# Performance work log

Hardware: AMD Instinct MI355X
Metric: run time of the kernel (lower is better)

## Reference

```python
import jax, jax.numpy as jnp
import numpy as np

N_SAMPLES = 524288
N_FEATURES = 64
N_GATES = 64
N_OUTPUTS = 8
BASE = N_FEATURES + 2                # X cols + constant-0 col + constant-1 col
MAX_CONN = BASE + N_GATES            # 130
TEMPERATURE = 1.0                    # forward() default
NEG = -1e9                           # mask value for not-yet-available slots


def setup_inputs() -> dict:
    key = jax.random.key(0)
    k1, k2, k3 = jax.random.split(key, 3)
    X = jax.random.uniform(k1, (N_SAMPLES, N_FEATURES), dtype=jnp.float32)
    gate_weights = jax.random.normal(k2, (N_GATES, MAX_CONN), dtype=jnp.float32) * 0.1
    output_weights = jax.random.normal(k3, (N_GATES, N_OUTPUTS), dtype=jnp.float32) * 0.1
    output_scale = jnp.ones((N_OUTPUTS,), dtype=jnp.float32)
    return {"X": X, "gate_weights": gate_weights,
            "output_weights": output_weights, "output_scale": output_scale}


def reference(X, gate_weights, output_weights, output_scale):
    n = X.shape[0]
    # available = [X | zeros | ones | gate slots]; gate slots filled sequentially
    buf = jnp.concatenate([
        X,
        jnp.zeros((n, 1), X.dtype),
        jnp.ones((n, 1), X.dtype),
        jnp.zeros((n, N_GATES), X.dtype),
    ], axis=1)                                            # [N, MAX_CONN]

    # Connection selection is data-independent: softmax over the first
    # (BASE + gate_idx) slots of each gate's weight row, then top-2.
    col_ids = jnp.arange(MAX_CONN)
    avail_mask = col_ids[None, :] < (BASE + jnp.arange(N_GATES))[:, None]
    logits = jnp.where(avail_mask, gate_weights / TEMPERATURE, NEG)
    probs = jax.nn.softmax(logits, axis=1)                # [n_gates, MAX_CONN]
    _, top2 = jax.lax.top_k(probs, 2)                     # [n_gates, 2]

    # Sequential NAND chain over a small fixed number of gates (structural loop).
    gate_outs = []
    for i in range(N_GATES):
        a = buf[:, top2[i, 0]]                            # [N]
        b = buf[:, top2[i, 1]]
        g = 1.0 - a * b                                   # continuous NAND
        gate_outs.append(g)
        buf = buf.at[:, BASE + i].set(g)

    gate_matrix = jnp.stack(gate_outs, axis=1)            # [N, n_gates]
    outputs = (gate_matrix @ output_weights) * output_scale
    return outputs
```

## Files before the change

kernel.cpp:

```cpp
#include <hip/hip_runtime.h>
#include <hip/hip_fp16.h>

#define N_SAMPLES 524288
#define N_FEATURES 64
#define N_GATES 64
#define N_OUTPUTS 8
#define BASE_COLS 66
#define MAX_CONN 130
#define NCOLS 131

#define TPB 256
#define NW 128
#define STR 129

#define WS_GIDX   0
#define WS_NCHK   512
#define WS_OWH2   1024
#define WS_ENT    4096

__device__ inline void top2_ins(float x, int j, float& v1, int& i1, float& v2, int& i2) {
    bool gt1 = (x > v1) || (x == v1 && j < i1);
    bool gt2 = (x > v2) || (x == v2 && j < i2);
    if (gt1) { v2 = v1; i2 = i1; v1 = x; i1 = j; }
    else if (gt2) { v2 = x; i2 = j; }
}

__global__ __launch_bounds__(64) void topk_prep_kernel(const float* __restrict__ gw,
                                                       int2* __restrict__ gidx) {
    const int i = blockIdx.x;
    const int l = threadIdx.x;
    const float* w = gw + i * MAX_CONN;
    const int avail = BASE_COLS + i;

    float v1 = -1e30f, v2 = -1e30f;
    int   i1 = 0x7fffffff, i2 = 0x7fffffff;
    for (int s = 0; s < 3; ++s) {
        int j = l + 64 * s;
        if (j < avail) top2_ins(w[j], j, v1, i1, v2, i2);
    }
    #pragma unroll
    for (int d = 1; d < 64; d <<= 1) {
        float ov1 = __shfl_xor(v1, d);
        int   oi1 = __shfl_xor(i1, d);
        float ov2 = __shfl_xor(v2, d);
        int   oi2 = __shfl_xor(i2, d);
        top2_ins(ov1, oi1, v1, i1, v2, i2);
        top2_ins(ov2, oi2, v1, i1, v2, i2);
    }
    if (l == 0) gidx[i] = make_int2(i1, i2);
}

__global__ __launch_bounds__(64) void plan_kernel(const int2* __restrict__ gidx,
                                                  const float* __restrict__ ow,
                                                  char* __restrict__ ws) {
    __shared__ int spa[N_GATES], spb[N_GATES];
    const int t = threadIdx.x;

    unsigned int* owh = (unsigned int*)(ws + WS_OWH2);
    int4* ent = (int4*)(ws + WS_ENT);
    int*  nchk = (int*)(ws + WS_NCHK);

    int2 p = gidx[t];
    spa[t] = p.x; spb[t] = p.y;

    #pragma unroll
    for (int o = 0; o < N_OUTPUTS; ++o) {
        unsigned short u = __half_as_ushort(__float2half(ow[t * N_OUTPUTS + o]));
        owh[t * N_OUTPUTS + o] = (unsigned int)u * 0x10001u;
    }
    if (t < N_OUTPUTS) owh[N_GATES * N_OUTPUTS + t] = 0u;

    __syncthreads();

    if (t == 0) {
        int i = 0, e = 0;
        while (i < N_GATES) {
            int cs = i;
            int limit = BASE_COLS + cs;
            while (i < N_GATES && spa[i] < limit && spb[i] < limit) ++i;
            for (int j = cs; j < i; ++j)
                ent[e++] = make_int4(spa[j] * STR, spb[j] * STR,
                                     (BASE_COLS + j) * STR, j);
            while (e & 7)
                ent[e++] = make_int4(64 * STR, 64 * STR, 130 * STR, N_GATES);
        }
        *nchk = e >> 3;
    }
}

__global__ __launch_bounds__(NW) void circuit_kernel(
    const float* __restrict__ X,
    const char*  __restrict__ ws,
    const float* __restrict__ scale,
    float*       __restrict__ out)
{
    __shared__ __half2 buf[NCOLS * STR];

    const int t = threadIdx.x;
    const long long s0 = (long long)blockIdx.x * TPB;

    const int4* ent = (const int4*)(ws + WS_ENT);
    const unsigned int* owh = (const unsigned int*)(ws + WS_OWH2);
    const int nc = *(const int*)(ws + WS_NCHK);

    const float4* Xv = (const float4*)(X + s0 * N_FEATURES);
    #pragma unroll
    for (int k = 0; k < 16; ++k) {
        int q  = k * NW + t;
        int c4 = q & 15;
        int j  = q >> 4;
        float4 va = Xv[(2 * j)     * 16 + c4];
        float4 vb = Xv[(2 * j + 1) * 16 + c4];
        int c = 4 * c4;
        buf[(c + 0) * STR + j] = __halves2half2(__float2half(va.x), __float2half(vb.x));
        buf[(c + 1) * STR + j] = __halves2half2(__float2half(va.y), __float2half(vb.y));
        buf[(c + 2) * STR + j] = __halves2half2(__float2half(va.z), __float2half(vb.z));
        buf[(c + 3) * STR + j] = __halves2half2(__float2half(va.w), __float2half(vb.w));
    }
    buf[64 * STR + t] = __halves2half2(__float2half(0.0f), __float2half(0.0f));
    buf[65 * STR + t] = __halves2half2(__float2half(1.0f), __float2half(1.0f));
    __syncthreads();

    const __half2 one2 = __halves2half2(__float2half(1.0f), __float2half(1.0f));
    __half2 acc[N_OUTPUTS];
    #pragma unroll
    for (int o = 0; o < N_OUTPUTS; ++o) acc[o] = __halves2half2(__float2half(0.0f), __float2half(0.0f));

    for (int c = 0; c < nc; ++c) {
        int4 E[8];
        #pragma unroll
        for (int j = 0; j < 8; ++j) E[j] = ent[c * 8 + j];

        __half2 av[8], bv[8];
        #pragma unroll
        for (int j = 0; j < 8; ++j) {
            av[j] = buf[E[j].x + t];
            bv[j] = buf[E[j].y + t];
        }
        __half2 gv[8];
        #pragma unroll
        for (int j = 0; j < 8; ++j) {
            gv[j] = __hfma2(__hneg2(av[j]), bv[j], one2);
            buf[E[j].z + t] = gv[j];
        }
        #pragma unroll
        for (int j = 0; j < 8; ++j) {
            const __half2* wrow = (const __half2*)(owh + E[j].w * N_OUTPUTS);
            #pragma unroll
            for (int o = 0; o < N_OUTPUTS; ++o)
                acc[o] = __hfma2(gv[j], wrow[o], acc[o]);
        }
    }

    float sc[N_OUTPUTS];
    #pragma unroll
    for (int o = 0; o < N_OUTPUTS; ++o) sc[o] = scale[o];

    float a0[N_OUTPUTS], a1[N_OUTPUTS];
    #pragma unroll
    for (int o = 0; o < N_OUTPUTS; ++o) {
        a0[o] = __low2float(acc[o])  * sc[o];
        a1[o] = __high2float(acc[o]) * sc[o];
    }
    float4* outv = (float4*)(out + (s0 + 2 * t) * N_OUTPUTS);
    outv[0] = make_float4(a0[0], a0[1], a0[2], a0[3]);
    outv[1] = make_float4(a0[4], a0[5], a0[6], a0[7]);
    outv[2] = make_float4(a1[0], a1[1], a1[2], a1[3]);
    outv[3] = make_float4(a1[4], a1[5], a1[6], a1[7]);
}

extern "C" void kernel_launch(void* const* d_in, const int* in_sizes, int n_in,
                              void* d_out, int out_size, void* d_ws, size_t ws_size,
                              hipStream_t stream) {
    const float* X     = (const float*)d_in[0];
    const float* gw    = (const float*)d_in[1];
    const float* ow    = (const float*)d_in[2];
    const float* scale = (const float*)d_in[3];
    float* out = (float*)d_out;

    char* ws = (char*)d_ws;
    int2* gidx = (int2*)(ws + WS_GIDX);

    topk_prep_kernel<<<N_GATES, 64, 0, stream>>>(gw, gidx);
    plan_kernel<<<1, 64, 0, stream>>>(gidx, ow, ws);

    int blocks = N_SAMPLES / TPB;
    circuit_kernel<<<blocks, NW, 0, stream>>>(X, ws, scale, out);
}
```

Baseline: 240.9 us.

## Compact LDS via liveness-based row allocation and prefetch chunk entries

The planner now reference-counts each column and assigns shared-memory rows only to live values. It reuses freed rows for later gate outputs and sends dead outputs to a scratch row, which shrinks the LDS footprint from 131 rows to 77 and should allow more resident blocks per CU. Unused X columns are skipped during staging. The circuit loop also double-buffers the next chunk's entry descriptors so their loads overlap the current chunk, at the cost of extra registers and a fixed row cap that could overflow if more values are live at once.

New measurement: 285.4 us. 18.5% more time.

```diff
diff --git a/kernel.cpp b/kernel.cpp
--- a/kernel.cpp
+++ b/kernel.cpp
@@ -7,16 +7,21 @@
 #define N_OUTPUTS 8
 #define BASE_COLS 66
 #define MAX_CONN 130
-#define NCOLS 131
 
 #define TPB 256
 #define NW 128
 #define STR 129
 
-#define WS_GIDX   0
-#define WS_NCHK   512
-#define WS_OWH2   1024
-#define WS_ENT    4096
+#define CAP_ROWS 77
+#define SCRATCH_ROW (CAP_ROWS - 1)
+#define DYN_LDS (CAP_ROWS * STR * 4)
+
+#define WS_GIDX 0
+#define WS_NCHK 1024
+#define WS_CROW 1056
+#define WS_XMAP 2048
+#define WS_OWH2 4096
+#define WS_ENT  8192
 
 __device__ inline void top2_ins(float x, int j, float& v1, int& i1, float& v2, int& i2) {
     bool gt1 = (x > v1) || (x == v1 && j < i1);
@@ -53,15 +58,13 @@
 __global__ __launch_bounds__(64) void plan_kernel(const int2* __restrict__ gidx,
                                                   const float* __restrict__ ow,
                                                   char* __restrict__ ws) {
-    __shared__ int spa[N_GATES], spb[N_GATES];
+    __shared__ int ga[N_GATES], gb[N_GATES];
+    __shared__ int refcnt[MAX_CONN], cmap[MAX_CONN];
     const int t = threadIdx.x;
 
     unsigned int* owh = (unsigned int*)(ws + WS_OWH2);
-    int4* ent = (int4*)(ws + WS_ENT);
-    int*  nchk = (int*)(ws + WS_NCHK);
-
     int2 p = gidx[t];
-    spa[t] = p.x; spb[t] = p.y;
+    ga[t] = p.x; gb[t] = p.y;
 
     #pragma unroll
     for (int o = 0; o < N_OUTPUTS; ++o) {
@@ -70,21 +73,48 @@
     }
     if (t < N_OUTPUTS) owh[N_GATES * N_OUTPUTS + t] = 0u;
 
+    refcnt[t] = 0; refcnt[t + 64] = 0;
+    cmap[t] = -1;  cmap[t + 64] = -1;
+    if (t < 2) { refcnt[128 + t] = 0; cmap[128 + t] = -1; }
     __syncthreads();
 
     if (t == 0) {
-        int i = 0, e = 0;
+        for (int i = 0; i < N_GATES; ++i) { refcnt[ga[i]]++; refcnt[gb[i]]++; }
+
+        int frees[CAP_ROWS]; int nfree = 0;
+        for (int r = SCRATCH_ROW - 1; r >= 0; --r) frees[nfree++] = r;
+
+        refcnt[64] += 1000000;
+        cmap[64] = frees[--nfree];
+        if (refcnt[65] > 0) cmap[65] = frees[--nfree];
+        for (int c = 0; c < 64; ++c) if (refcnt[c] > 0) cmap[c] = frees[--nfree];
+
+        int* xmap = (int*)(ws + WS_XMAP);
+        for (int c = 0; c < 64; ++c) xmap[c] = (cmap[c] >= 0) ? cmap[c] * STR : -1;
+        *(int2*)(ws + WS_CROW) =
+            make_int2(cmap[64] * STR, (cmap[65] >= 0) ? cmap[65] * STR : -1);
+
+        int4* ent = (int4*)(ws + WS_ENT);
+        const int zoff = cmap[64] * STR;
+        int e = 0, i = 0;
         while (i < N_GATES) {
-            int cs = i;
-            int limit = BASE_COLS + cs;
-            while (i < N_GATES && spa[i] < limit && spb[i] < limit) ++i;
-            for (int j = cs; j < i; ++j)
-                ent[e++] = make_int4(spa[j] * STR, spb[j] * STR,
-                                     (BASE_COLS + j) * STR, j);
-            while (e & 7)
-                ent[e++] = make_int4(64 * STR, 64 * STR, 130 * STR, N_GATES);
-        }
-        *nchk = e >> 3;
+            int cs = i, limit = BASE_COLS + cs;
+            while (i < N_GATES && ga[i] < limit && gb[i] < limit) ++i;
+            for (int j = cs; j < i; ++j) {
+                int ca = ga[j], cb = gb[j];
+                int ra = cmap[ca] * STR, rb = cmap[cb] * STR;
+                if (--refcnt[ca] == 0 && nfree < SCRATCH_ROW) frees[nfree++] = cmap[ca];
+                if (--refcnt[cb] == 0 && nfree < SCRATCH_ROW) frees[nfree++] = cmap[cb];
+                int ro = SCRATCH_ROW;
+                if (refcnt[BASE_COLS + j] > 0 && nfree > 0) ro = frees[--nfree];
+                cmap[BASE_COLS + j] = ro;
+                ent[e++] = make_int4(ra, rb, ro * STR, j);
+            }
+            while (e & 7) ent[e++] = make_int4(zoff, zoff, SCRATCH_ROW * STR, N_GATES);
+        }
+        *(int*)(ws + WS_NCHK) = e >> 3;
+        for (int j = 0; j < 8; ++j)
+            ent[e++] = make_int4(zoff, zoff, SCRATCH_ROW * STR, N_GATES);
     }
 }
 
@@ -94,7 +124,7 @@
     const float* __restrict__ scale,
     float*       __restrict__ out)
 {
-    __shared__ __half2 buf[NCOLS * STR];
+    extern __shared__ __half2 buf[];
 
     const int t = threadIdx.x;
     const long long s0 = (long long)blockIdx.x * TPB;
@@ -102,23 +132,25 @@
     const int4* ent = (const int4*)(ws + WS_ENT);
     const unsigned int* owh = (const unsigned int*)(ws + WS_OWH2);
     const int nc = *(const int*)(ws + WS_NCHK);
+    const int2 crow = *(const int2*)(ws + WS_CROW);
+
+    const int c4 = t & 15;
+    const int jb = t >> 4;
+    const int4 xm = ((const int4*)(ws + WS_XMAP))[c4];
 
     const float4* Xv = (const float4*)(X + s0 * N_FEATURES);
     #pragma unroll
     for (int k = 0; k < 16; ++k) {
-        int q  = k * NW + t;
-        int c4 = q & 15;
-        int j  = q >> 4;
+        int j = 8 * k + jb;
         float4 va = Xv[(2 * j)     * 16 + c4];
         float4 vb = Xv[(2 * j + 1) * 16 + c4];
-        int c = 4 * c4;
-        buf[(c + 0) * STR + j] = __halves2half2(__float2half(va.x), __float2half(vb.x));
-        buf[(c + 1) * STR + j] = __halves2half2(__float2half(va.y), __float2half(vb.y));
-        buf[(c + 2) * STR + j] = __halves2half2(__float2half(va.z), __float2half(vb.z));
-        buf[(c + 3) * STR + j] = __halves2half2(__float2half(va.w), __float2half(vb.w));
-    }
-    buf[64 * STR + t] = __halves2half2(__float2half(0.0f), __float2half(0.0f));
-    buf[65 * STR + t] = __halves2half2(__float2half(1.0f), __float2half(1.0f));
+        if (xm.x >= 0) buf[xm.x + j] = __halves2half2(__float2half(va.x), __float2half(vb.x));
+        if (xm.y >= 0) buf[xm.y + j] = __halves2half2(__float2half(va.y), __float2half(vb.y));
+        if (xm.z >= 0) buf[xm.z + j] = __halves2half2(__float2half(va.z), __float2half(vb.z));
+        if (xm.w >= 0) buf[xm.w + j] = __halves2half2(__float2half(va.w), __float2half(vb.w));
+    }
+    buf[crow.x + t] = __halves2half2(__float2half(0.0f), __float2half(0.0f));
+    if (crow.y >= 0) buf[crow.y + t] = __halves2half2(__float2half(1.0f), __float2half(1.0f));
     __syncthreads();
 
     const __half2 one2 = __halves2half2(__float2half(1.0f), __float2half(1.0f));
@@ -126,10 +158,14 @@
     #pragma unroll
     for (int o = 0; o < N_OUTPUTS; ++o) acc[o] = __halves2half2(__float2half(0.0f), __float2half(0.0f));
 
+    int4 E[8];
+    #pragma unroll
+    for (int j = 0; j < 8; ++j) E[j] = ent[j];
+
     for (int c = 0; c < nc; ++c) {
-        int4 E[8];
-        #pragma unroll
-        for (int j = 0; j < 8; ++j) E[j] = ent[c * 8 + j];
+        int4 En[8];
+        #pragma unroll
+        for (int j = 0; j < 8; ++j) En[j] = ent[(c + 1) * 8 + j];
 
         __half2 av[8], bv[8];
         #pragma unroll
@@ -150,6 +186,8 @@
             for (int o = 0; o < N_OUTPUTS; ++o)
                 acc[o] = __hfma2(gv[j], wrow[o], acc[o]);
         }
+        #pragma unroll
+        for (int j = 0; j < 8; ++j) E[j] = En[j];
     }
 
     float sc[N_OUTPUTS];
@@ -185,5 +223,5 @@
     plan_kernel<<<1, 64, 0, stream>>>(gidx, ow, ws);
 
     int blocks = N_SAMPLES / TPB;
-    circuit_kernel<<<blocks, NW, 0, stream>>>(X, ws, scale, out);
-}
+    circuit_kernel<<<blocks, NW, DYN_LDS, stream>>>(X, ws, scale, out);
+}
```
